# Performance work log

Measured on AMD Instinct MI355X. Metric: run time of the kernel, lower is better.

Reference implementation:

```python
import jax, jax.numpy as jnp
import numpy as np

N_BUCKET, EPB, K, TAU = 4, 4, 2, 1.0
C, H = 512, 1024
E = N_BUCKET * EPB
B, T = 2, 1024

def _l2norm(v):
    # matches F.normalize(dim=-1): v / max(||v||, 1e-12)
    return v / jnp.maximum(jnp.linalg.norm(v, axis=-1, keepdims=True), 1e-12)

def setup_inputs() -> dict:
    key = jax.random.key(0)
    ks = jax.random.split(key, 8)
    s = 1.0 / np.sqrt(C).astype(np.float32)
    sh = 1.0 / np.sqrt(H).astype(np.float32)
    return {
        "x": jax.random.normal(ks[0], (B, T, C), jnp.float32),
        "op_id": jax.random.randint(ks[1], (B, T), 0, N_BUCKET),
        "expert_key": jax.random.normal(ks[2], (N_BUCKET, EPB, C), jnp.float32) * s,
        "sW1": jax.random.normal(ks[3], (C, H), jnp.float32) * s,
        "sb1": jnp.zeros((H,), jnp.float32),
        "sW2": jax.random.normal(ks[4], (H, C), jnp.float32) * sh,
        "sb2": jnp.zeros((C,), jnp.float32),
        "eW1": jax.random.normal(ks[5], (E, C, H), jnp.float32) * s,
        "eb1": jnp.zeros((E, H), jnp.float32),
        "eW2": jax.random.normal(ks[6], (E, H, C), jnp.float32) * sh,
        "eb2": jnp.zeros((E, C), jnp.float32),
        "gate_logit": jnp.float32(-2.0),
    }

def reference(x, op_id, expert_key, sW1, sb1, sW2, sb2, eW1, eb1, eW2, eb2, gate_logit):
    Bb, Tt, Cc = x.shape
    # --- HierKVRouter ---
    bucket = jnp.clip(op_id, 0, N_BUCKET - 1)                 # (B,T)
    h_n = _l2norm(x)                                          # (B,T,C)
    keys = _l2norm(expert_key)                                # (nb,epb,C)
    keys_bt = keys[bucket]                                    # (B,T,epb,C) gather
    score = jnp.einsum('btc,btec->bte', h_n, keys_bt) / max(TAU, 1e-6)
    probs_local = jax.nn.softmax(score, axis=-1)              # (B,T,epb)
    topv, local = jax.lax.top_k(probs_local, K)               # (B,T,K)
    w = topv / (jnp.sum(topv, axis=-1, keepdims=True) + 1e-9) # combine weights
    gid = bucket[..., None] * EPB + local                     # (B,T,K) global ids
    # --- dispatch / expert MLP / combine ---
    flat_in = jnp.broadcast_to(x[:, :, None, :], (Bb, Tt, K, Cc)).reshape(-1, Cc)
    flat_gid = gid.reshape(-1)                                # (B*T*K,)
    flat_w = w.reshape(-1)                                    # (B*T*K,)
    out = jnp.zeros_like(flat_in)
    for e in range(E):  # fixed small expert count; masked dense = exact math of torch boolean-mask loop
        mask = (flat_gid == e)[:, None]
        h1 = jax.nn.relu(flat_in @ eW1[e] + eb1[e])
        oe = h1 @ eW2[e] + eb2[e]
        out = out + jnp.where(mask, oe * flat_w[:, None], 0.0)
    moe_out = out.reshape(Bb, Tt, K, Cc).sum(axis=2)          # (B,T,C)
    # --- shared dense FFN + gated combine ---
    dense = jax.nn.relu(x @ sW1 + sb1) @ sW2 + sb2
    y = dense + jax.nn.sigmoid(gate_logit) * moe_out
    return y
```

## Files before the change

### kernel.cpp

```cpp
#include <hip/hip_runtime.h>
#include <hip/hip_bf16.h>
#include <math.h>

#define C_DIM 512
#define H_DIM 1024
#define NTOK  2048
#define NSLOT 4096
#define NROWS 6144
#define MAXT128 64
#define MAXT64  112
#define NBG1 512

typedef __attribute__((ext_vector_type(8))) short short8;
typedef __attribute__((ext_vector_type(4))) float floatx4;
typedef __attribute__((address_space(3))) void as3_void;
typedef const __attribute__((address_space(1))) void as1_cvoid;

__device__ __forceinline__ void gload_lds16(const void* g, void* l){
  __builtin_amdgcn_global_load_lds((as1_cvoid*)g, (as3_void*)l, 16, 0, 0);
}

__device__ __forceinline__ unsigned short f2b(float f){
  unsigned int u = __float_as_uint(f);
  unsigned int r = (u + 0x7FFFu + ((u >> 16) & 1u)) >> 16;
  return (unsigned short)r;
}

__device__ __forceinline__ void transpose_tile(const float* __restrict__ in,
                                               unsigned short* __restrict__ out,
                                               int K, int N, int n0, int k0,
                                               int tid, float* tile){
  int tx = tid & 15, ty = tid >> 4;
  #pragma unroll
  for (int i = 0; i < 8; i++){
    int k = ty + 16 * i;
    float4 v = *reinterpret_cast<const float4*>(in + (size_t)(k0 + k) * N + n0 + tx * 4);
    tile[(4*tx + 0) * 129 + k] = v.x;
    tile[(4*tx + 1) * 129 + k] = v.y;
    tile[(4*tx + 2) * 129 + k] = v.z;
    tile[(4*tx + 3) * 129 + k] = v.w;
  }
  __syncthreads();
  int wt = tid & 31, wr = tid >> 5;
  #pragma unroll
  for (int i = 0; i < 8; i++){
    int n = wr + 8 * i;
    float4 v = *reinterpret_cast<const float4*>(&tile[n * 129 + 4 * wt]);
    ushort4 o;
    o.x = f2b(v.x); o.y = f2b(v.y); o.z = f2b(v.z); o.w = f2b(v.w);
    *reinterpret_cast<ushort4*>(out + (size_t)(n0 + n) * K + k0 + 4 * wt) = o;
  }
}

__global__ __launch_bounds__(256) void k_router(const float* __restrict__ x,
                                                const int* __restrict__ op_id,
                                                const float* __restrict__ ekey,
                                                unsigned short* __restrict__ Xb,
                                                int* __restrict__ gids,
                                                float* __restrict__ wv){
  int t = blockIdx.x * 4 + (threadIdx.x >> 6);
  int lane = threadIdx.x & 63;
  const float* xr = x + (size_t)t * C_DIM;
  {
    const float4* xr4 = reinterpret_cast<const float4*>(xr);
    float4 a = xr4[lane * 2], b = xr4[lane * 2 + 1];
    short8 o;
    o[0] = (short)f2b(a.x); o[1] = (short)f2b(a.y); o[2] = (short)f2b(a.z); o[3] = (short)f2b(a.w);
    o[4] = (short)f2b(b.x); o[5] = (short)f2b(b.y); o[6] = (short)f2b(b.z); o[7] = (short)f2b(b.w);
    *reinterpret_cast<short8*>(Xb + (size_t)t * C_DIM + lane * 8) = o;
  }
  float xs[8];
  float xn2 = 0.f;
  #pragma unroll
  for (int i = 0; i < 8; i++){ float v = xr[lane + 64*i]; xs[i] = v; xn2 += v*v; }
  #pragma unroll
  for (int o = 32; o; o >>= 1) xn2 += __shfl_xor(xn2, o, 64);
  int bucket = min(max(op_id[t], 0), 3);
  float xn = fmaxf(sqrtf(xn2), 1e-12f);
  float pr[4];
  #pragma unroll
  for (int e = 0; e < 4; e++){
    const float* kr = ekey + ((size_t)bucket * 4 + e) * C_DIM;
    float dot = 0.f, kn2 = 0.f;
    #pragma unroll
    for (int i = 0; i < 8; i++){ float kv = kr[lane + 64*i]; dot += xs[i]*kv; kn2 += kv*kv; }
    #pragma unroll
    for (int o = 32; o; o >>= 1){ dot += __shfl_xor(dot, o, 64); kn2 += __shfl_xor(kn2, o, 64); }
    float kn = fmaxf(sqrtf(kn2), 1e-12f);
    pr[e] = dot / (xn * kn);
  }
  float mx = fmaxf(fmaxf(pr[0], pr[1]), fmaxf(pr[2], pr[3]));
  float Z = 0.f;
  #pragma unroll
  for (int e = 0; e < 4; e++){ pr[e] = expf(pr[e] - mx); Z += pr[e]; }
  #pragma unroll
  for (int e = 0; e < 4; e++) pr[e] /= Z;
  int i0 = 0;
  #pragma unroll
  for (int e = 1; e < 4; e++) if (pr[e] > pr[i0]) i0 = e;
  int i1 = (i0 == 0) ? 1 : 0;
  #pragma unroll
  for (int e = 0; e < 4; e++) if (e != i0 && e != i1 && pr[e] > pr[i1]) i1 = e;
  float v0 = pr[i0], v1 = pr[i1];
  float wsum = v0 + v1 + 1e-9f;
  if (lane == 0){
    gids[2*t]   = bucket * 4 + i0;
    gids[2*t+1] = bucket * 4 + i1;
    wv[2*t]   = v0 / wsum;
    wv[2*t+1] = v1 / wsum;
  }
}

__global__ __launch_bounds__(256) void k_sortw1(const int* __restrict__ gids,
                                                const float* __restrict__ wv,
                                                const float* __restrict__ gate,
                                                const float* __restrict__ sW1,
                                                const float* __restrict__ eW1,
                                                unsigned short* __restrict__ sW1t,
                                                unsigned short* __restrict__ eW1t,
                                                int* __restrict__ inv,
                                                int* __restrict__ rowTok,
                                                float* __restrict__ rowW,
                                                int* __restrict__ tiles128,
                                                int* __restrict__ tiles64){
  __shared__ __align__(16) char smem[33280];
  const int bid = blockIdx.x;
  const int tid = threadIdx.x;

  if (bid == 0){
    int (*hist)[16] = (int(*)[16])smem;
    int* off = (int*)(smem + 16384);
    float sig = 1.f / (1.f + expf(-gate[0]));
    int h[16], g_[16];
    #pragma unroll
    for (int e = 0; e < 16; e++) h[e] = 0;
    int base = tid * 16;
    #pragma unroll
    for (int s = 0; s < 16; s++){ g_[s] = gids[base + s]; h[g_[s]]++; }
    #pragma unroll
    for (int e = 0; e < 16; e++) hist[tid][e] = h[e];
    __syncthreads();
    for (int d = 1; d < 256; d <<= 1){
      int v[16];
      if (tid >= d){
        #pragma unroll
        for (int e = 0; e < 16; e++) v[e] = hist[tid - d][e];
      }
      __syncthreads();
      if (tid >= d){
        #pragma unroll
        for (int e = 0; e < 16; e++) hist[tid][e] += v[e];
      }
      __syncthreads();
    }
    if (tid == 0){
      off[0] = 0;
      for (int e = 0; e < 16; e++) off[e+1] = off[e] + hist[255][e];
    }
    __syncthreads();
    int c[16];
    #pragma unroll
    for (int e = 0; e < 16; e++) c[e] = off[e] + hist[tid][e] - h[e];
    #pragma unroll
    for (int s = 0; s < 16; s++){
      int slot = base + s;
      int g = g_[s];
      int pos = c[g]++;
      inv[slot] = pos;
      rowTok[NTOK + pos] = slot >> 1;
      rowW[NTOK + pos] = sig * wv[slot];
    }
    for (int r = tid; r < NTOK; r += 256){ rowTok[r] = r; rowW[r] = 1.0f; }
    __syncthreads();
    if (tid == 0){
      int nt = 0;
      for (int r0 = 0; r0 < NTOK; r0 += 128){
        tiles128[nt*3] = r0; tiles128[nt*3+1] = 128; tiles128[nt*3+2] = 16; nt++;
      }
      for (int e = 0; e < 16; e++){
        int cc = off[e+1] - off[e];
        for (int r0 = 0; r0 < cc; r0 += 128){
          tiles128[nt*3] = NTOK + off[e] + r0;
          tiles128[nt*3+1] = min(128, cc - r0);
          tiles128[nt*3+2] = e;
          nt++;
        }
      }
      for (int i = nt; i < MAXT128; i++){ tiles128[i*3] = 0; tiles128[i*3+1] = 0; tiles128[i*3+2] = 0; }
      nt = 0;
      for (int r0 = 0; r0 < NTOK; r0 += 64){
        tiles64[nt*3] = r0; tiles64[nt*3+1] = 64; tiles64[nt*3+2] = 16; nt++;
      }
      for (int e = 0; e < 16; e++){
        int cc = off[e+1] - off[e];
        for (int r0 = 0; r0 < cc; r0 += 64){
          tiles64[nt*3] = NTOK + off[e] + r0;
          tiles64[nt*3+1] = min(64, cc - r0);
          tiles64[nt*3+2] = e;
          nt++;
        }
      }
      for (int i = nt; i < MAXT64; i++){ tiles64[i*3] = 0; tiles64[i*3+1] = 0; tiles64[i*3+2] = 0; }
    }
    return;
  }

  int tb = bid - 1;
  int mat = tb >> 6, tl = tb & 63;
  const float* in  = (mat < 16) ? eW1 + (size_t)mat * C_DIM * H_DIM : sW1;
  unsigned short* out = (mat < 16) ? eW1t + (size_t)mat * C_DIM * H_DIM : sW1t;
  transpose_tile(in, out, C_DIM, H_DIM, (tl & 15) * 64, (tl >> 4) * 128, tid, (float*)smem);
}

__global__ __launch_bounds__(256) void k_g1w2(const unsigned short* __restrict__ A,
                                              const unsigned short* __restrict__ BtE,
                                              const unsigned short* __restrict__ BtS,
                                              const float* __restrict__ biasE,
                                              const float* __restrict__ biasS,
                                              const int* __restrict__ rowTok,
                                              const int* __restrict__ tiles,
                                              unsigned short* __restrict__ outB,
                                              const float* __restrict__ sW2,
                                              const float* __restrict__ eW2,
                                              unsigned short* __restrict__ sW2t,
                                              unsigned short* __restrict__ eW2t){
  __shared__ __align__(16) char smem[33024];
  const int bx = blockIdx.x;
  const int tid = threadIdx.x;

  if (bx >= NBG1){
    int wi = bx - NBG1;
    int mat = wi >> 6, tl = wi & 63;
    const float* in  = (mat < 16) ? eW2 + (size_t)mat * H_DIM * C_DIM : sW2;
    unsigned short* out = (mat < 16) ? eW2t + (size_t)mat * H_DIM * C_DIM : sW2t;
    transpose_tile(in, out, H_DIM, C_DIM, (tl & 7) * 64, (tl >> 3) * 128, tid, (float*)smem);
    return;
  }

  constexpr int KDIM = C_DIM, NDIM = H_DIM;
  const int tileId = bx >> 3;
  const int rows = tiles[tileId*3+1];
  if (rows == 0) return;
  const int row0 = tiles[tileId*3];
  const int eid  = tiles[tileId*3+2];
  const unsigned short* Bt = (eid < 16) ? (BtE + (size_t)eid * NDIM * KDIM) : BtS;
  const float* bias = (eid < 16) ? (biasE + eid * NDIM) : biasS;
  const int n0 = (bx & 7) * 128;

  char* As = smem;
  char* Bs = smem + 16384;

  const int lane = tid & 63;
  const int wid = tid >> 6;
  const int wm = wid >> 1, wn = wid & 1;
  const int l15 = lane & 15, lhi = lane >> 4;

  int aRow[4], aOff[4], bRow[4], bOff[4];
  #pragma unroll
  for (int j = 0; j < 4; j++){
    int c = j * 256 + tid;
    int i = c >> 3, op = c & 7;
    int o = op ^ (i & 7);
    int ie = min(i, rows - 1);
    aRow[j] = rowTok[row0 + ie];
    aOff[j] = o * 8;
    bRow[j] = n0 + i;
    bOff[j] = o * 8;
  }

  floatx4 acc[4][4] = {};
  constexpr int NT = KDIM / 64;

  for (int kt = 0; kt < NT; ++kt){
    #pragma unroll
    for (int j = 0; j < 4; j++)
      gload_lds16(A + (size_t)aRow[j] * KDIM + kt * 64 + aOff[j],
                  As + (j * 256 + tid) * 16);
    #pragma unroll
    for (int j = 0; j < 4; j++)
      gload_lds16(Bt + (size_t)bRow[j] * KDIM + kt * 64 + bOff[j],
                  Bs + (j * 256 + tid) * 16);
    __syncthreads();
    #pragma unroll
    for (int kk = 0; kk < 2; ++kk){
      short8 a[4], b[4];
      #pragma unroll
      for (int m = 0; m < 4; m++){
        int rr = wm * 64 + m * 16 + l15;
        a[m] = *reinterpret_cast<const short8*>(
            As + rr * 128 + ((kk * 64 + lhi * 16) ^ ((rr & 7) << 4)));
      }
      #pragma unroll
      for (int n = 0; n < 4; n++){
        int rr = wn * 64 + n * 16 + l15;
        b[n] = *reinterpret_cast<const short8*>(
            Bs + rr * 128 + ((kk * 64 + lhi * 16) ^ ((rr & 7) << 4)));
      }
      #pragma unroll
      for (int m = 0; m < 4; m++)
        #pragma unroll
        for (int n = 0; n < 4; n++)
          acc[m][n] = __builtin_amdgcn_mfma_f32_16x16x32_bf16(a[m], b[n], acc[m][n], 0, 0, 0);
    }
    __syncthreads();
  }

  #pragma unroll
  for (int m = 0; m < 4; m++){
    #pragma unroll
    for (int n = 0; n < 4; n++){
      int gcol = n0 + wn * 64 + n * 16 + l15;
      float bv = bias[gcol];
      #pragma unroll
      for (int q = 0; q < 4; q++){
        int ri = wm * 64 + m * 16 + lhi * 4 + q;
        if (ri < rows){
          float v = fmaxf(acc[m][n][q] + bv, 0.f);
          outB[(size_t)(row0 + ri) * NDIM + gcol] = f2b(v);
        }
      }
    }
  }
}

template<int BMT, int KDIM, int NDIM>
__global__ __launch_bounds__(256) void k_gemm2(const unsigned short* __restrict__ A,
                                               const unsigned short* __restrict__ BtE,
                                               const unsigned short* __restrict__ BtS,
                                               const float* __restrict__ biasE,
                                               const float* __restrict__ biasS,
                                               const float* __restrict__ rowW,
                                               const int* __restrict__ tiles,
                                               float* __restrict__ outF){
  const int tileId = blockIdx.x;
  const int rows = tiles[tileId*3+1];
  if (rows == 0) return;
  const int row0 = tiles[tileId*3];
  const int eid  = tiles[tileId*3+2];
  const unsigned short* Bt = (eid < 16) ? (BtE + (size_t)eid * NDIM * KDIM) : BtS;
  const float* bias = (eid < 16) ? (biasE + eid * NDIM) : biasS;
  const int n0 = blockIdx.y * 128;

  constexpr int MREP = BMT / 32;
  constexpr int AISS = BMT * 8 / 256;

  __shared__ __align__(16) unsigned short As[2][BMT * 64];
  __shared__ __align__(16) unsigned short Bs[2][128 * 64];

  const int tid = threadIdx.x;
  const int lane = tid & 63;
  const int wid = tid >> 6;
  const int wm = wid >> 1, wn = wid & 1;
  const int l15 = lane & 15, lhi = lane >> 4;

  int aRow[AISS], aOff[AISS];
  #pragma unroll
  for (int j = 0; j < AISS; j++){
    int c = j * 256 + tid;
    int i = c >> 3, op = c & 7;
    int o = op ^ (i & 7);
    int ie = min(i, rows - 1);
    aRow[j] = row0 + ie;
    aOff[j] = o * 8;
  }
  int bRow[4], bOff[4];
  #pragma unroll
  for (int j = 0; j < 4; j++){
    int c = j * 256 + tid;
    int i = c >> 3, op = c & 7;
    int o = op ^ (i & 7);
    bRow[j] = n0 + i;
    bOff[j] = o * 8;
  }

  auto STAGE = [&](int buf, int kt){
    #pragma unroll
    for (int j = 0; j < AISS; j++)
      gload_lds16(A + (size_t)aRow[j] * KDIM + kt * 64 + aOff[j],
                  (char*)&As[buf][0] + (j * 256 + tid) * 16);
    #pragma unroll
    for (int j = 0; j < 4; j++)
      gload_lds16(Bt + (size_t)bRow[j] * KDIM + kt * 64 + bOff[j],
                  (char*)&Bs[buf][0] + (j * 256 + tid) * 16);
  };

  floatx4 acc[MREP][4] = {};
  constexpr int NT = KDIM / 64;

  STAGE(0, 0);
  for (int kt = 0; kt < NT; ++kt){
    const int cur = kt & 1;
    if (kt + 1 < NT){
      STAGE(cur ^ 1, kt + 1);
      asm volatile("s_waitcnt vmcnt(6)" ::: "memory");
    } else {
      asm volatile("s_waitcnt vmcnt(0)" ::: "memory");
    }
    __builtin_amdgcn_s_barrier();
    asm volatile("" ::: "memory");
    #pragma unroll
    for (int kk = 0; kk < 2; ++kk){
      short8 a[MREP], b[4];
      #pragma unroll
      for (int m = 0; m < MREP; m++){
        int rr = wm * (BMT/2) + m * 16 + l15;
        a[m] = *reinterpret_cast<const short8*>(
            (char*)&As[cur][0] + rr * 128 + ((kk * 64 + lhi * 16) ^ ((rr & 7) << 4)));
      }
      #pragma unroll
      for (int n = 0; n < 4; n++){
        int rr = wn * 64 + n * 16 + l15;
        b[n] = *reinterpret_cast<const short8*>(
            (char*)&Bs[cur][0] + rr * 128 + ((kk * 64 + lhi * 16) ^ ((rr & 7) << 4)));
      }
      #pragma unroll
      for (int m = 0; m < MREP; m++)
        #pragma unroll
        for (int n = 0; n < 4; n++)
          acc[m][n] = __builtin_amdgcn_mfma_f32_16x16x32_bf16(a[m], b[n], acc[m][n], 0, 0, 0);
    }
    asm volatile("" ::: "memory");
    __builtin_amdgcn_s_barrier();
  }

  #pragma unroll
  for (int m = 0; m < MREP; m++){
    #pragma unroll
    for (int n = 0; n < 4; n++){
      int gcol = n0 + wn * 64 + n * 16 + l15;
      float bv = bias[gcol];
      #pragma unroll
      for (int q = 0; q < 4; q++){
        int ri = wm * (BMT/2) + m * 16 + lhi * 4 + q;
        if (ri < rows){
          float v = (acc[m][n][q] + bv) * rowW[row0 + ri];
          outF[(size_t)(row0 + ri) * NDIM + gcol] = v;
        }
      }
    }
  }
}

__global__ __launch_bounds__(256) void k_combine(const float* __restrict__ O,
                                                 const int* __restrict__ inv,
                                                 float* __restrict__ y){
  int q = blockIdx.x * 256 + threadIdx.x;
  int t = q >> 7, c4 = q & 127;
  const float4* Of = reinterpret_cast<const float4*>(O);
  float4 d  = Of[(size_t)t * 128 + c4];
  int p0 = inv[2*t], p1 = inv[2*t+1];
  float4 o0 = Of[(size_t)(NTOK + p0) * 128 + c4];
  float4 o1 = Of[(size_t)(NTOK + p1) * 128 + c4];
  float4 r;
  r.x = d.x + o0.x + o1.x;
  r.y = d.y + o0.y + o1.y;
  r.z = d.z + o0.z + o1.z;
  r.w = d.w + o0.w + o1.w;
  reinterpret_cast<float4*>(y)[q] = r;
}

extern "C" void kernel_launch(void* const* d_in, const int* in_sizes, int n_in,
                              void* d_out, int out_size, void* d_ws, size_t ws_size,
                              hipStream_t stream){
  const float* x    = (const float*)d_in[0];
  const int*   opid = (const int*)d_in[1];
  const float* ekey = (const float*)d_in[2];
  const float* sW1  = (const float*)d_in[3];
  const float* sb1  = (const float*)d_in[4];
  const float* sW2  = (const float*)d_in[5];
  const float* sb2  = (const float*)d_in[6];
  const float* eW1  = (const float*)d_in[7];
  const float* eb1  = (const float*)d_in[8];
  const float* eW2  = (const float*)d_in[9];
  const float* eb2  = (const float*)d_in[10];
  const float* gate = (const float*)d_in[11];
  float* y = (float*)d_out;

  char* ws = (char*)d_ws;
  size_t off = 0;
  auto alloc = [&](size_t bytes) -> char* {
    char* p = ws + off; off += (bytes + 255) & ~(size_t)255; return p;
  };
  unsigned short* Xb   = (unsigned short*)alloc((size_t)NTOK * C_DIM * 2);
  unsigned short* sW1t = (unsigned short*)alloc((size_t)H_DIM * C_DIM * 2);
  unsigned short* sW2t = (unsigned short*)alloc((size_t)C_DIM * H_DIM * 2);
  unsigned short* eW1t = (unsigned short*)alloc((size_t)16 * H_DIM * C_DIM * 2);
  unsigned short* eW2t = (unsigned short*)alloc((size_t)16 * C_DIM * H_DIM * 2);
  unsigned short* H1   = (unsigned short*)alloc((size_t)NROWS * H_DIM * 2);
  float* O      = (float*)alloc((size_t)NROWS * C_DIM * 4);
  float* wv     = (float*)alloc((size_t)NSLOT * 4);
  int*   gids   = (int*)alloc((size_t)NSLOT * 4);
  int*   inv    = (int*)alloc((size_t)NSLOT * 4);
  int*   rowTok = (int*)alloc((size_t)NROWS * 4);
  float* rowW   = (float*)alloc((size_t)NROWS * 4);
  int*   tiles128 = (int*)alloc((size_t)MAXT128 * 3 * 4);
  int*   tiles64  = (int*)alloc((size_t)MAXT64 * 3 * 4);

  k_router<<<512, 256, 0, stream>>>(x, opid, ekey, Xb, gids, wv);
  k_sortw1<<<1 + 1088, 256, 0, stream>>>(gids, wv, gate, sW1, eW1, sW1t, eW1t,
                                         inv, rowTok, rowW, tiles128, tiles64);
  k_g1w2<<<NBG1 + 1088, 256, 0, stream>>>(Xb, eW1t, sW1t, eb1, sb1, rowTok, tiles128, H1,
                                          sW2, eW2, sW2t, eW2t);
  k_gemm2<64, H_DIM, C_DIM><<<dim3(MAXT64, C_DIM/128), 256, 0, stream>>>(
      H1, eW2t, sW2t, eb2, sb2, rowW, tiles64, O);
  k_combine<<<1024, 256, 0, stream>>>(O, inv, y);
}
```

Baseline: 79.58 us.

## Retile both GEMMs to 128-row tiles, widen gemm1 blocks, store gemm2 output as bf16

The first expert GEMM now runs 512-thread blocks that each cover 256 output columns instead of 128, with a block index remap that groups neighbouring column blocks of the same row tile. The weight-transpose blocks fused into that kernel are adapted to 512 threads. The second GEMM drops its 64-row double-buffered variant and reuses the 128-row tile list with a single-buffered loop, and it writes its output as bf16. The combine kernel then reads half the bytes. This cuts tile-list construction, the number of gemm2 blocks and intermediate traffic, but loses load/compute overlap in gemm2 and adds bf16 rounding error before the final sum.

```diff
diff --git a/kernel.cpp b/kernel.cpp
--- a/kernel.cpp
+++ b/kernel.cpp
@@ -8,8 +8,8 @@
 #define NSLOT 4096
 #define NROWS 6144
 #define MAXT128 64
-#define MAXT64  112
-#define NBG1 512
+#define NBG1 256
+#define NW2T 1088
 
 typedef __attribute__((ext_vector_type(8))) short short8;
 typedef __attribute__((ext_vector_type(4))) float floatx4;
@@ -24,6 +24,9 @@
   unsigned int u = __float_as_uint(f);
   unsigned int r = (u + 0x7FFFu + ((u >> 16) & 1u)) >> 16;
   return (unsigned short)r;
+}
+__device__ __forceinline__ float b2f(unsigned short s){
+  return __uint_as_float(((unsigned int)s) << 16);
 }
 
 __device__ __forceinline__ void transpose_tile(const float* __restrict__ in,
@@ -45,6 +48,32 @@
   #pragma unroll
   for (int i = 0; i < 8; i++){
     int n = wr + 8 * i;
+    float4 v = *reinterpret_cast<const float4*>(&tile[n * 129 + 4 * wt]);
+    ushort4 o;
+    o.x = f2b(v.x); o.y = f2b(v.y); o.z = f2b(v.z); o.w = f2b(v.w);
+    *reinterpret_cast<ushort4*>(out + (size_t)(n0 + n) * K + k0 + 4 * wt) = o;
+  }
+}
+
+__device__ __forceinline__ void transpose_tile512(const float* __restrict__ in,
+                                                  unsigned short* __restrict__ out,
+                                                  int K, int N, int n0, int k0,
+                                                  int tid, float* tile){
+  int tx = tid & 15, ty = tid >> 4;
+  #pragma unroll
+  for (int i = 0; i < 4; i++){
+    int k = ty + 32 * i;
+    float4 v = *reinterpret_cast<const float4*>(in + (size_t)(k0 + k) * N + n0 + tx * 4);
+    tile[(4*tx + 0) * 129 + k] = v.x;
+    tile[(4*tx + 1) * 129 + k] = v.y;
+    tile[(4*tx + 2) * 129 + k] = v.z;
+    tile[(4*tx + 3) * 129 + k] = v.w;
+  }
+  __syncthreads();
+  int wt = tid & 31, wr = tid >> 5;
+  #pragma unroll
+  for (int i = 0; i < 4; i++){
+    int n = wr + 16 * i;
     float4 v = *reinterpret_cast<const float4*>(&tile[n * 129 + 4 * wt]);
     ushort4 o;
     o.x = f2b(v.x); o.y = f2b(v.y); o.z = f2b(v.z); o.w = f2b(v.w);
@@ -121,8 +150,7 @@
                                                 int* __restrict__ inv,
                                                 int* __restrict__ rowTok,
                                                 float* __restrict__ rowW,
-                                                int* __restrict__ tiles128,
-                                                int* __restrict__ tiles64){
+                                                int* __restrict__ tiles128){
   __shared__ __align__(16) char smem[33280];
   const int bid = blockIdx.x;
   const int tid = threadIdx.x;
@@ -187,20 +215,6 @@
         }
       }
       for (int i = nt; i < MAXT128; i++){ tiles128[i*3] = 0; tiles128[i*3+1] = 0; tiles128[i*3+2] = 0; }
-      nt = 0;
-      for (int r0 = 0; r0 < NTOK; r0 += 64){
-        tiles64[nt*3] = r0; tiles64[nt*3+1] = 64; tiles64[nt*3+2] = 16; nt++;
-      }
-      for (int e = 0; e < 16; e++){
-        int cc = off[e+1] - off[e];
-        for (int r0 = 0; r0 < cc; r0 += 64){
-          tiles64[nt*3] = NTOK + off[e] + r0;
-          tiles64[nt*3+1] = min(64, cc - r0);
-          tiles64[nt*3+2] = e;
-          nt++;
-        }
-      }
-      for (int i = nt; i < MAXT64; i++){ tiles64[i*3] = 0; tiles64[i*3+1] = 0; tiles64[i*3+2] = 0; }
     }
     return;
   }
@@ -212,7 +226,7 @@
   transpose_tile(in, out, C_DIM, H_DIM, (tl & 15) * 64, (tl >> 4) * 128, tid, (float*)smem);
 }
 
-__global__ __launch_bounds__(256) void k_g1w2(const unsigned short* __restrict__ A,
+__global__ __launch_bounds__(512) void k_g1w2(const unsigned short* __restrict__ A,
                                               const unsigned short* __restrict__ BtE,
                                               const unsigned short* __restrict__ BtS,
                                               const float* __restrict__ biasE,
@@ -224,7 +238,7 @@
                                               const float* __restrict__ eW2,
                                               unsigned short* __restrict__ sW2t,
                                               unsigned short* __restrict__ eW2t){
-  __shared__ __align__(16) char smem[33024];
+  __shared__ __align__(16) char smem[49152];
   const int bx = blockIdx.x;
   const int tid = threadIdx.x;
 
@@ -233,53 +247,58 @@
     int mat = wi >> 6, tl = wi & 63;
     const float* in  = (mat < 16) ? eW2 + (size_t)mat * H_DIM * C_DIM : sW2;
     unsigned short* out = (mat < 16) ? eW2t + (size_t)mat * H_DIM * C_DIM : sW2t;
-    transpose_tile(in, out, H_DIM, C_DIM, (tl & 7) * 64, (tl >> 3) * 128, tid, (float*)smem);
+    transpose_tile512(in, out, H_DIM, C_DIM, (tl & 7) * 64, (tl >> 3) * 128, tid, (float*)smem);
     return;
   }
 
   constexpr int KDIM = C_DIM, NDIM = H_DIM;
-  const int tileId = bx >> 3;
+  const int tileId = (bx & 7) + 8 * (bx >> 5);
+  const int nb = (bx >> 3) & 3;
   const int rows = tiles[tileId*3+1];
   if (rows == 0) return;
   const int row0 = tiles[tileId*3];
   const int eid  = tiles[tileId*3+2];
   const unsigned short* Bt = (eid < 16) ? (BtE + (size_t)eid * NDIM * KDIM) : BtS;
   const float* bias = (eid < 16) ? (biasE + eid * NDIM) : biasS;
-  const int n0 = (bx & 7) * 128;
+  const int n0 = nb * 256;
 
   char* As = smem;
   char* Bs = smem + 16384;
 
   const int lane = tid & 63;
   const int wid = tid >> 6;
-  const int wm = wid >> 1, wn = wid & 1;
+  const int wm = wid >> 2, wn = wid & 3;
   const int l15 = lane & 15, lhi = lane >> 4;
 
-  int aRow[4], aOff[4], bRow[4], bOff[4];
-  #pragma unroll
-  for (int j = 0; j < 4; j++){
-    int c = j * 256 + tid;
+  int aRow[2], aOff[2], bRow[4], bOff[4];
+  #pragma unroll
+  for (int j = 0; j < 2; j++){
+    int c = j * 512 + tid;
     int i = c >> 3, op = c & 7;
     int o = op ^ (i & 7);
     int ie = min(i, rows - 1);
     aRow[j] = rowTok[row0 + ie];
     aOff[j] = o * 8;
+  }
+  #pragma unroll
+  for (int j = 0; j < 4; j++){
+    int c = j * 512 + tid;
+    int i = c >> 3, op = c & 7;
+    int o = op ^ (i & 7);
     bRow[j] = n0 + i;
     bOff[j] = o * 8;
   }
 
   floatx4 acc[4][4] = {};
-  constexpr int NT = KDIM / 64;
-
-  for (int kt = 0; kt < NT; ++kt){
-    #pragma unroll
-    for (int j = 0; j < 4; j++)
+  for (int kt = 0; kt < KDIM / 64; ++kt){
+    #pragma unroll
+    for (int j = 0; j < 2; j++)
       gload_lds16(A + (size_t)aRow[j] * KDIM + kt * 64 + aOff[j],
-                  As + (j * 256 + tid) * 16);
+                  As + (j * 512 + tid) * 16);
     #pragma unroll
     for (int j = 0; j < 4; j++)
       gload_lds16(Bt + (size_t)bRow[j] * KDIM + kt * 64 + bOff[j],
-                  Bs + (j * 256 + tid) * 16);
+                  Bs + (j * 512 + tid) * 16);
     __syncthreads();
     #pragma unroll
     for (int kk = 0; kk < 2; ++kk){
@@ -323,7 +342,6 @@
   }
 }
 
-template<int BMT, int KDIM, int NDIM>
 __global__ __launch_bounds__(256) void k_gemm2(const unsigned short* __restrict__ A,
                                                const unsigned short* __restrict__ BtE,
                                                const unsigned short* __restrict__ BtS,
@@ -331,21 +349,21 @@
                                                const float* __restrict__ biasS,
                                                const float* __restrict__ rowW,
                                                const int* __restrict__ tiles,
-                                               float* __restrict__ outF){
-  const int tileId = blockIdx.x;
+                                               unsigned short* __restrict__ outB){
+  constexpr int KDIM = H_DIM, NDIM = C_DIM;
+  const int bx = blockIdx.x;
+  const int tileId = (bx & 7) + 8 * (bx >> 5);
+  const int nb = (bx >> 3) & 3;
   const int rows = tiles[tileId*3+1];
   if (rows == 0) return;
   const int row0 = tiles[tileId*3];
   const int eid  = tiles[tileId*3+2];
   const unsigned short* Bt = (eid < 16) ? (BtE + (size_t)eid * NDIM * KDIM) : BtS;
   const float* bias = (eid < 16) ? (biasE + eid * NDIM) : biasS;
-  const int n0 = blockIdx.y * 128;
-
-  constexpr int MREP = BMT / 32;
-  constexpr int AISS = BMT * 8 / 256;
-
-  __shared__ __align__(16) unsigned short As[2][BMT * 64];
-  __shared__ __align__(16) unsigned short Bs[2][128 * 64];
+  const int n0 = nb * 128;
+
+  __shared__ __align__(16) unsigned short As[128 * 64];
+  __shared__ __align__(16) unsigned short Bs[128 * 64];
 
   const int tid = threadIdx.x;
   const int lane = tid & 63;
@@ -353,109 +371,87 @@
   const int wm = wid >> 1, wn = wid & 1;
   const int l15 = lane & 15, lhi = lane >> 4;
 
-  int aRow[AISS], aOff[AISS];
-  #pragma unroll
-  for (int j = 0; j < AISS; j++){
+  int aRow[4], aOff[4], bRow[4], bOff[4];
+  #pragma unroll
+  for (int j = 0; j < 4; j++){
     int c = j * 256 + tid;
     int i = c >> 3, op = c & 7;
     int o = op ^ (i & 7);
     int ie = min(i, rows - 1);
     aRow[j] = row0 + ie;
     aOff[j] = o * 8;
-  }
-  int bRow[4], bOff[4];
-  #pragma unroll
-  for (int j = 0; j < 4; j++){
-    int c = j * 256 + tid;
-    int i = c >> 3, op = c & 7;
-    int o = op ^ (i & 7);
     bRow[j] = n0 + i;
     bOff[j] = o * 8;
   }
 
-  auto STAGE = [&](int buf, int kt){
-    #pragma unroll
-    for (int j = 0; j < AISS; j++)
+  floatx4 acc[4][4] = {};
+  for (int kt = 0; kt < KDIM / 64; ++kt){
+    #pragma unroll
+    for (int j = 0; j < 4; j++)
       gload_lds16(A + (size_t)aRow[j] * KDIM + kt * 64 + aOff[j],
-                  (char*)&As[buf][0] + (j * 256 + tid) * 16);
+                  (char*)As + (j * 256 + tid) * 16);
     #pragma unroll
     for (int j = 0; j < 4; j++)
       gload_lds16(Bt + (size_t)bRow[j] * KDIM + kt * 64 + bOff[j],
-                  (char*)&Bs[buf][0] + (j * 256 + tid) * 16);
-  };
-
-  floatx4 acc[MREP][4] = {};
-  constexpr int NT = KDIM / 64;
-
-  STAGE(0, 0);
-  for (int kt = 0; kt < NT; ++kt){
-    const int cur = kt & 1;
-    if (kt + 1 < NT){
-      STAGE(cur ^ 1, kt + 1);
-      asm volatile("s_waitcnt vmcnt(6)" ::: "memory");
-    } else {
-      asm volatile("s_waitcnt vmcnt(0)" ::: "memory");
-    }
-    __builtin_amdgcn_s_barrier();
-    asm volatile("" ::: "memory");
+                  (char*)Bs + (j * 256 + tid) * 16);
+    __syncthreads();
     #pragma unroll
     for (int kk = 0; kk < 2; ++kk){
-      short8 a[MREP], b[4];
-      #pragma unroll
-      for (int m = 0; m < MREP; m++){
-        int rr = wm * (BMT/2) + m * 16 + l15;
+      short8 a[4], b[4];
+      #pragma unroll
+      for (int m = 0; m < 4; m++){
+        int rr = wm * 64 + m * 16 + l15;
         a[m] = *reinterpret_cast<const short8*>(
-            (char*)&As[cur][0] + rr * 128 + ((kk * 64 + lhi * 16) ^ ((rr & 7) << 4)));
+            (char*)As + rr * 128 + ((kk * 64 + lhi * 16) ^ ((rr & 7) << 4)));
       }
       #pragma unroll
       for (int n = 0; n < 4; n++){
         int rr = wn * 64 + n * 16 + l15;
         b[n] = *reinterpret_cast<const short8*>(
-            (char*)&Bs[cur][0] + rr * 128 + ((kk * 64 + lhi * 16) ^ ((rr & 7) << 4)));
-      }
-      #pragma unroll
-      for (int m = 0; m < MREP; m++)
+            (char*)Bs + rr * 128 + ((kk * 64 + lhi * 16) ^ ((rr & 7) << 4)));
+      }
+      #pragma unroll
+      for (int m = 0; m < 4; m++)
         #pragma unroll
         for (int n = 0; n < 4; n++)
           acc[m][n] = __builtin_amdgcn_mfma_f32_16x16x32_bf16(a[m], b[n], acc[m][n], 0, 0, 0);
     }
-    asm volatile("" ::: "memory");
-    __builtin_amdgcn_s_barrier();
-  }
-
-  #pragma unroll
-  for (int m = 0; m < MREP; m++){
+    __syncthreads();
+  }
+
+  #pragma unroll
+  for (int m = 0; m < 4; m++){
     #pragma unroll
     for (int n = 0; n < 4; n++){
       int gcol = n0 + wn * 64 + n * 16 + l15;
       float bv = bias[gcol];
       #pragma unroll
       for (int q = 0; q < 4; q++){
-        int ri = wm * (BMT/2) + m * 16 + lhi * 4 + q;
+        int ri = wm * 64 + m * 16 + lhi * 4 + q;
         if (ri < rows){
           float v = (acc[m][n][q] + bv) * rowW[row0 + ri];
-          outF[(size_t)(row0 + ri) * NDIM + gcol] = v;
+          outB[(size_t)(row0 + ri) * NDIM + gcol] = f2b(v);
         }
       }
     }
   }
 }
 
-__global__ __launch_bounds__(256) void k_combine(const float* __restrict__ O,
+__global__ __launch_bounds__(256) void k_combine(const unsigned short* __restrict__ O,
                                                  const int* __restrict__ inv,
                                                  float* __restrict__ y){
   int q = blockIdx.x * 256 + threadIdx.x;
   int t = q >> 7, c4 = q & 127;
-  const float4* Of = reinterpret_cast<const float4*>(O);
-  float4 d  = Of[(size_t)t * 128 + c4];
+  const ushort4* O4 = reinterpret_cast<const ushort4*>(O);
+  ushort4 d  = O4[(size_t)t * 128 + c4];
   int p0 = inv[2*t], p1 = inv[2*t+1];
-  float4 o0 = Of[(size_t)(NTOK + p0) * 128 + c4];
-  float4 o1 = Of[(size_t)(NTOK + p1) * 128 + c4];
+  ushort4 o0 = O4[(size_t)(NTOK + p0) * 128 + c4];
+  ushort4 o1 = O4[(size_t)(NTOK + p1) * 128 + c4];
   float4 r;
-  r.x = d.x + o0.x + o1.x;
-  r.y = d.y + o0.y + o1.y;
-  r.z = d.z + o0.z + o1.z;
-  r.w = d.w + o0.w + o1.w;
+  r.x = b2f(d.x) + b2f(o0.x) + b2f(o1.x);
+  r.y = b2f(d.y) + b2f(o0.y) + b2f(o1.y);
+  r.z = b2f(d.z) + b2f(o0.z) + b2f(o1.z);
+  r.w = b2f(d.w) + b2f(o0.w) + b2f(o1.w);
   reinterpret_cast<float4*>(y)[q] = r;
 }
 
@@ -487,21 +483,19 @@
   unsigned short* eW1t = (unsigned short*)alloc((size_t)16 * H_DIM * C_DIM * 2);
   unsigned short* eW2t = (unsigned short*)alloc((size_t)16 * C_DIM * H_DIM * 2);
   unsigned short* H1   = (unsigned short*)alloc((size_t)NROWS * H_DIM * 2);
-  float* O      = (float*)alloc((size_t)NROWS * C_DIM * 4);
+  unsigned short* O    = (unsigned short*)alloc((size_t)NROWS * C_DIM * 2);
   float* wv     = (float*)alloc((size_t)NSLOT * 4);
   int*   gids   = (int*)alloc((size_t)NSLOT * 4);
   int*   inv    = (int*)alloc((size_t)NSLOT * 4);
   int*   rowTok = (int*)alloc((size_t)NROWS * 4);
   float* rowW   = (float*)alloc((size_t)NROWS * 4);
   int*   tiles128 = (int*)alloc((size_t)MAXT128 * 3 * 4);
-  int*   tiles64  = (int*)alloc((size_t)MAXT64 * 3 * 4);
 
   k_router<<<512, 256, 0, stream>>>(x, opid, ekey, Xb, gids, wv);
   k_sortw1<<<1 + 1088, 256, 0, stream>>>(gids, wv, gate, sW1, eW1, sW1t, eW1t,
-                                         inv, rowTok, rowW, tiles128, tiles64);
-  k_g1w2<<<NBG1 + 1088, 256, 0, stream>>>(Xb, eW1t, sW1t, eb1, sb1, rowTok, tiles128, H1,
+                                         inv, rowTok, rowW, tiles128);
+  k_g1w2<<<NBG1 + NW2T, 512, 0, stream>>>(Xb, eW1t, sW1t, eb1, sb1, rowTok, tiles128, H1,
                                           sW2, eW2, sW2t, eW2t);
-  k_gemm2<64, H_DIM, C_DIM><<<dim3(MAXT64, C_DIM/128), 256, 0, stream>>>(
-      H1, eW2t, sW2t, eb2, sb2, rowW, tiles64, O);
+  k_gemm2<<<256, 256, 0, stream>>>(H1, eW2t, sW2t, eb2, sb2, rowW, tiles128, O);
   k_combine<<<1024, 256, 0, stream>>>(O, inv, y);
 }
```

New measurement: 85.28 us. 1.07x slower.

## Reschedule MoE pipeline stages to overlap dense and expert GEMMs with weight transposes

Applied to the files above, without the earlier changes.

Reorganizes the kernel chain so the W1 transposes run alongside the router, the shared dense GEMM1 runs alongside the sort and the W2 transposes, and the dense GEMM2 runs alongside the expert GEMM1. The expert GEMM2 now uses a separate kernel with 128-row tiles in place of the double-buffered 64-row gemm2. The goal is less dependency serialization and better fill of the GPU across stages. The cost is that the expert GEMM2 loses the double-buffered load pipeline, and the dense GEMM2 now waits on the same launch as the expert GEMM1.

```diff
diff --git a/kernel.cpp b/kernel.cpp
--- a/kernel.cpp
+++ b/kernel.cpp
@@ -7,9 +7,7 @@
 #define NTOK  2048
 #define NSLOT 4096
 #define NROWS 6144
-#define MAXT128 64
-#define MAXT64  112
-#define NBG1 512
+#define MAXTE 48
 
 typedef __attribute__((ext_vector_type(8))) short short8;
 typedef __attribute__((ext_vector_type(4))) float floatx4;
@@ -52,14 +50,119 @@
   }
 }
 
-__global__ __launch_bounds__(256) void k_router(const float* __restrict__ x,
-                                                const int* __restrict__ op_id,
-                                                const float* __restrict__ ekey,
-                                                unsigned short* __restrict__ Xb,
-                                                int* __restrict__ gids,
-                                                float* __restrict__ wv){
-  int t = blockIdx.x * 4 + (threadIdx.x >> 6);
-  int lane = threadIdx.x & 63;
+template<bool GATHER, bool RELU, bool OUTBF, bool WEIGHTED, int KDIM, int NDIM>
+__device__ __forceinline__ void gemm_tile(const unsigned short* __restrict__ A,
+                                          const unsigned short* __restrict__ Bt,
+                                          const float* __restrict__ bias,
+                                          const int* __restrict__ rowTok,
+                                          const float* __restrict__ rowW,
+                                          int row0, int rows, int n0,
+                                          int tid, char* smem,
+                                          unsigned short* __restrict__ outB,
+                                          float* __restrict__ outF){
+  char* As = smem;
+  char* Bs = smem + 16384;
+  const int lane = tid & 63;
+  const int wid = tid >> 6;
+  const int wm = wid >> 1, wn = wid & 1;
+  const int l15 = lane & 15, lhi = lane >> 4;
+
+  int aRow[4], aOff[4], bRow[4], bOff[4];
+  #pragma unroll
+  for (int j = 0; j < 4; j++){
+    int c = j * 256 + tid;
+    int i = c >> 3, op = c & 7;
+    int o = op ^ (i & 7);
+    int ie = min(i, rows - 1);
+    aRow[j] = GATHER ? rowTok[row0 + ie] : (row0 + ie);
+    aOff[j] = o * 8;
+    bRow[j] = n0 + i;
+    bOff[j] = o * 8;
+  }
+
+  floatx4 acc[4][4] = {};
+  for (int kt = 0; kt < KDIM / 64; ++kt){
+    #pragma unroll
+    for (int j = 0; j < 4; j++)
+      gload_lds16(A + (size_t)aRow[j] * KDIM + kt * 64 + aOff[j],
+                  As + (j * 256 + tid) * 16);
+    #pragma unroll
+    for (int j = 0; j < 4; j++)
+      gload_lds16(Bt + (size_t)bRow[j] * KDIM + kt * 64 + bOff[j],
+                  Bs + (j * 256 + tid) * 16);
+    __syncthreads();
+    #pragma unroll
+    for (int kk = 0; kk < 2; ++kk){
+      short8 a[4], b[4];
+      #pragma unroll
+      for (int m = 0; m < 4; m++){
+        int rr = wm * 64 + m * 16 + l15;
+        a[m] = *reinterpret_cast<const short8*>(
+            As + rr * 128 + ((kk * 64 + lhi * 16) ^ ((rr & 7) << 4)));
+      }
+      #pragma unroll
+      for (int n = 0; n < 4; n++){
+        int rr = wn * 64 + n * 16 + l15;
+        b[n] = *reinterpret_cast<const short8*>(
+            Bs + rr * 128 + ((kk * 64 + lhi * 16) ^ ((rr & 7) << 4)));
+      }
+      #pragma unroll
+      for (int m = 0; m < 4; m++)
+        #pragma unroll
+        for (int n = 0; n < 4; n++)
+          acc[m][n] = __builtin_amdgcn_mfma_f32_16x16x32_bf16(a[m], b[n], acc[m][n], 0, 0, 0);
+    }
+    __syncthreads();
+  }
+
+  #pragma unroll
+  for (int m = 0; m < 4; m++){
+    #pragma unroll
+    for (int n = 0; n < 4; n++){
+      int gcol = n0 + wn * 64 + n * 16 + l15;
+      float bv = bias[gcol];
+      #pragma unroll
+      for (int q = 0; q < 4; q++){
+        int ri = wm * 64 + m * 16 + lhi * 4 + q;
+        if (ri < rows){
+          float v = acc[m][n][q] + bv;
+          if constexpr (OUTBF){
+            if (RELU) v = fmaxf(v, 0.f);
+            outB[(size_t)(row0 + ri) * NDIM + gcol] = f2b(v);
+          } else {
+            if constexpr (WEIGHTED) v *= rowW[row0 + ri];
+            outF[(size_t)(row0 + ri) * NDIM + gcol] = v;
+          }
+        }
+      }
+    }
+  }
+}
+
+__global__ __launch_bounds__(256) void k_prep(const float* __restrict__ x,
+                                              const int* __restrict__ op_id,
+                                              const float* __restrict__ ekey,
+                                              const float* __restrict__ sW1,
+                                              const float* __restrict__ eW1,
+                                              unsigned short* __restrict__ Xb,
+                                              unsigned short* __restrict__ sW1t,
+                                              unsigned short* __restrict__ eW1t,
+                                              int* __restrict__ gids,
+                                              float* __restrict__ wv){
+  __shared__ __align__(16) float tile[64 * 129];
+  const int bid = blockIdx.x;
+  const int tid = threadIdx.x;
+
+  if (bid >= 512){
+    int tb = bid - 512;
+    int mat = tb >> 6, tl = tb & 63;
+    const float* in  = (mat < 16) ? eW1 + (size_t)mat * C_DIM * H_DIM : sW1;
+    unsigned short* out = (mat < 16) ? eW1t + (size_t)mat * C_DIM * H_DIM : sW1t;
+    transpose_tile(in, out, C_DIM, H_DIM, (tl & 15) * 64, (tl >> 4) * 128, tid, tile);
+    return;
+  }
+  int t = bid * 4 + (tid >> 6);
+  int lane = tid & 63;
   const float* xr = x + (size_t)t * C_DIM;
   {
     const float4* xr4 = reinterpret_cast<const float4*>(xr);
@@ -111,19 +214,22 @@
   }
 }
 
-__global__ __launch_bounds__(256) void k_sortw1(const int* __restrict__ gids,
-                                                const float* __restrict__ wv,
-                                                const float* __restrict__ gate,
-                                                const float* __restrict__ sW1,
-                                                const float* __restrict__ eW1,
-                                                unsigned short* __restrict__ sW1t,
-                                                unsigned short* __restrict__ eW1t,
-                                                int* __restrict__ inv,
-                                                int* __restrict__ rowTok,
-                                                float* __restrict__ rowW,
-                                                int* __restrict__ tiles128,
-                                                int* __restrict__ tiles64){
-  __shared__ __align__(16) char smem[33280];
+__global__ __launch_bounds__(256) void k_sg1d(const int* __restrict__ gids,
+                                              const float* __restrict__ wv,
+                                              const float* __restrict__ gate,
+                                              int* __restrict__ inv,
+                                              int* __restrict__ rowTok,
+                                              float* __restrict__ rowW,
+                                              int* __restrict__ tilesE,
+                                              const unsigned short* __restrict__ Xb,
+                                              const unsigned short* __restrict__ sW1t,
+                                              const float* __restrict__ sb1,
+                                              unsigned short* __restrict__ H1,
+                                              const float* __restrict__ sW2,
+                                              const float* __restrict__ eW2,
+                                              unsigned short* __restrict__ sW2t,
+                                              unsigned short* __restrict__ eW2t){
+  __shared__ __align__(16) char smem[33024];
   const int bid = blockIdx.x;
   const int tid = threadIdx.x;
 
@@ -170,275 +276,83 @@
       rowTok[NTOK + pos] = slot >> 1;
       rowW[NTOK + pos] = sig * wv[slot];
     }
-    for (int r = tid; r < NTOK; r += 256){ rowTok[r] = r; rowW[r] = 1.0f; }
     __syncthreads();
     if (tid == 0){
       int nt = 0;
-      for (int r0 = 0; r0 < NTOK; r0 += 128){
-        tiles128[nt*3] = r0; tiles128[nt*3+1] = 128; tiles128[nt*3+2] = 16; nt++;
-      }
       for (int e = 0; e < 16; e++){
         int cc = off[e+1] - off[e];
         for (int r0 = 0; r0 < cc; r0 += 128){
-          tiles128[nt*3] = NTOK + off[e] + r0;
-          tiles128[nt*3+1] = min(128, cc - r0);
-          tiles128[nt*3+2] = e;
+          tilesE[nt*3] = NTOK + off[e] + r0;
+          tilesE[nt*3+1] = min(128, cc - r0);
+          tilesE[nt*3+2] = e;
           nt++;
         }
       }
-      for (int i = nt; i < MAXT128; i++){ tiles128[i*3] = 0; tiles128[i*3+1] = 0; tiles128[i*3+2] = 0; }
-      nt = 0;
-      for (int r0 = 0; r0 < NTOK; r0 += 64){
-        tiles64[nt*3] = r0; tiles64[nt*3+1] = 64; tiles64[nt*3+2] = 16; nt++;
-      }
-      for (int e = 0; e < 16; e++){
-        int cc = off[e+1] - off[e];
-        for (int r0 = 0; r0 < cc; r0 += 64){
-          tiles64[nt*3] = NTOK + off[e] + r0;
-          tiles64[nt*3+1] = min(64, cc - r0);
-          tiles64[nt*3+2] = e;
-          nt++;
-        }
-      }
-      for (int i = nt; i < MAXT64; i++){ tiles64[i*3] = 0; tiles64[i*3+1] = 0; tiles64[i*3+2] = 0; }
+      for (int i = nt; i < MAXTE; i++){ tilesE[i*3] = 0; tilesE[i*3+1] = 0; tilesE[i*3+2] = 0; }
     }
     return;
   }
-
-  int tb = bid - 1;
+  if (bid <= 128){
+    int g = bid - 1;
+    gemm_tile<false, true, true, false, C_DIM, H_DIM>(
+        Xb, sW1t, sb1, nullptr, nullptr,
+        (g >> 3) * 128, 128, (g & 7) * 128, tid, smem, H1, nullptr);
+    return;
+  }
+  int tb = bid - 129;
   int mat = tb >> 6, tl = tb & 63;
-  const float* in  = (mat < 16) ? eW1 + (size_t)mat * C_DIM * H_DIM : sW1;
-  unsigned short* out = (mat < 16) ? eW1t + (size_t)mat * C_DIM * H_DIM : sW1t;
-  transpose_tile(in, out, C_DIM, H_DIM, (tl & 15) * 64, (tl >> 4) * 128, tid, (float*)smem);
-}
-
-__global__ __launch_bounds__(256) void k_g1w2(const unsigned short* __restrict__ A,
-                                              const unsigned short* __restrict__ BtE,
-                                              const unsigned short* __restrict__ BtS,
-                                              const float* __restrict__ biasE,
-                                              const float* __restrict__ biasS,
-                                              const int* __restrict__ rowTok,
-                                              const int* __restrict__ tiles,
-                                              unsigned short* __restrict__ outB,
-                                              const float* __restrict__ sW2,
-                                              const float* __restrict__ eW2,
-                                              unsigned short* __restrict__ sW2t,
-                                              unsigned short* __restrict__ eW2t){
+  const float* in  = (mat < 16) ? eW2 + (size_t)mat * H_DIM * C_DIM : sW2;
+  unsigned short* out = (mat < 16) ? eW2t + (size_t)mat * H_DIM * C_DIM : sW2t;
+  transpose_tile(in, out, H_DIM, C_DIM, (tl & 7) * 64, (tl >> 3) * 128, tid, (float*)smem);
+}
+
+__global__ __launch_bounds__(256) void k_g1e_g2d(const unsigned short* __restrict__ Xb,
+                                                 const unsigned short* __restrict__ eW1t,
+                                                 const float* __restrict__ eb1,
+                                                 const int* __restrict__ rowTok,
+                                                 const int* __restrict__ tilesE,
+                                                 unsigned short* __restrict__ H1,
+                                                 const unsigned short* __restrict__ sW2t,
+                                                 const float* __restrict__ sb2,
+                                                 float* __restrict__ O){
   __shared__ __align__(16) char smem[33024];
-  const int bx = blockIdx.x;
+  const int bid = blockIdx.x;
   const int tid = threadIdx.x;
 
-  if (bx >= NBG1){
-    int wi = bx - NBG1;
-    int mat = wi >> 6, tl = wi & 63;
-    const float* in  = (mat < 16) ? eW2 + (size_t)mat * H_DIM * C_DIM : sW2;
-    unsigned short* out = (mat < 16) ? eW2t + (size_t)mat * H_DIM * C_DIM : sW2t;
-    transpose_tile(in, out, H_DIM, C_DIM, (tl & 7) * 64, (tl >> 3) * 128, tid, (float*)smem);
+  if (bid < MAXTE * 8){
+    const int tileId = bid >> 3;
+    const int rows = tilesE[tileId*3+1];
+    if (rows == 0) return;
+    const int row0 = tilesE[tileId*3];
+    const int eid  = tilesE[tileId*3+2];
+    gemm_tile<true, true, true, false, C_DIM, H_DIM>(
+        Xb, eW1t + (size_t)eid * H_DIM * C_DIM, eb1 + eid * H_DIM, rowTok, nullptr,
+        row0, rows, (bid & 7) * 128, tid, smem, H1, nullptr);
     return;
   }
-
-  constexpr int KDIM = C_DIM, NDIM = H_DIM;
-  const int tileId = bx >> 3;
-  const int rows = tiles[tileId*3+1];
+  int g = bid - MAXTE * 8;
+  gemm_tile<false, false, false, false, H_DIM, C_DIM>(
+      H1, sW2t, sb2, nullptr, nullptr,
+      (g >> 2) * 128, 128, (g & 3) * 128, tid, smem, nullptr, O);
+}
+
+__global__ __launch_bounds__(256) void k_g2e(const unsigned short* __restrict__ H1,
+                                             const unsigned short* __restrict__ eW2t,
+                                             const float* __restrict__ eb2,
+                                             const float* __restrict__ rowW,
+                                             const int* __restrict__ tilesE,
+                                             float* __restrict__ O){
+  __shared__ __align__(16) char smem[33024];
+  const int bid = blockIdx.x;
+  const int tid = threadIdx.x;
+  const int tileId = bid >> 2;
+  const int rows = tilesE[tileId*3+1];
   if (rows == 0) return;
-  const int row0 = tiles[tileId*3];
-  const int eid  = tiles[tileId*3+2];
-  const unsigned short* Bt = (eid < 16) ? (BtE + (size_t)eid * NDIM * KDIM) : BtS;
-  const float* bias = (eid < 16) ? (biasE + eid * NDIM) : biasS;
-  const int n0 = (bx & 7) * 128;
-
-  char* As = smem;
-  char* Bs = smem + 16384;
-
-  const int lane = tid & 63;
-  const int wid = tid >> 6;
-  const int wm = wid >> 1, wn = wid & 1;
-  const int l15 = lane & 15, lhi = lane >> 4;
-
-  int aRow[4], aOff[4], bRow[4], bOff[4];
-  #pragma unroll
-  for (int j = 0; j < 4; j++){
-    int c = j * 256 + tid;
-    int i = c >> 3, op = c & 7;
-    int o = op ^ (i & 7);
-    int ie = min(i, rows - 1);
-    aRow[j] = rowTok[row0 + ie];
-    aOff[j] = o * 8;
-    bRow[j] = n0 + i;
-    bOff[j] = o * 8;
-  }
-
-  floatx4 acc[4][4] = {};
-  constexpr int NT = KDIM / 64;
-
-  for (int kt = 0; kt < NT; ++kt){
-    #pragma unroll
-    for (int j = 0; j < 4; j++)
-      gload_lds16(A + (size_t)aRow[j] * KDIM + kt * 64 + aOff[j],
-                  As + (j * 256 + tid) * 16);
-    #pragma unroll
-    for (int j = 0; j < 4; j++)
-      gload_lds16(Bt + (size_t)bRow[j] * KDIM + kt * 64 + bOff[j],
-                  Bs + (j * 256 + tid) * 16);
-    __syncthreads();
-    #pragma unroll
-    for (int kk = 0; kk < 2; ++kk){
-      short8 a[4], b[4];
-      #pragma unroll
-      for (int m = 0; m < 4; m++){
-        int rr = wm * 64 + m * 16 + l15;
-        a[m] = *reinterpret_cast<const short8*>(
-            As + rr * 128 + ((kk * 64 + lhi * 16) ^ ((rr & 7) << 4)));
-      }
-      #pragma unroll
-      for (int n = 0; n < 4; n++){
-        int rr = wn * 64 + n * 16 + l15;
-        b[n] = *reinterpret_cast<const short8*>(
-            Bs + rr * 128 + ((kk * 64 + lhi * 16) ^ ((rr & 7) << 4)));
-      }
-      #pragma unroll
-      for (int m = 0; m < 4; m++)
-        #pragma unroll
-        for (int n = 0; n < 4; n++)
-          acc[m][n] = __builtin_amdgcn_mfma_f32_16x16x32_bf16(a[m], b[n], acc[m][n], 0, 0, 0);
-    }
-    __syncthreads();
-  }
-
-  #pragma unroll
-  for (int m = 0; m < 4; m++){
-    #pragma unroll
-    for (int n = 0; n < 4; n++){
-      int gcol = n0 + wn * 64 + n * 16 + l15;
-      float bv = bias[gcol];
-      #pragma unroll
-      for (int q = 0; q < 4; q++){
-        int ri = wm * 64 + m * 16 + lhi * 4 + q;
-        if (ri < rows){
-          float v = fmaxf(acc[m][n][q] + bv, 0.f);
-          outB[(size_t)(row0 + ri) * NDIM + gcol] = f2b(v);
-        }
-      }
-    }
-  }
-}
-
-template<int BMT, int KDIM, int NDIM>
-__global__ __launch_bounds__(256) void k_gemm2(const unsigned short* __restrict__ A,
-                                               const unsigned short* __restrict__ BtE,
-                                               const unsigned short* __restrict__ BtS,
-                                               const float* __restrict__ biasE,
-                                               const float* __restrict__ biasS,
-                                               const float* __restrict__ rowW,
-                                               const int* __restrict__ tiles,
-                                               float* __restrict__ outF){
-  const int tileId = blockIdx.x;
-  const int rows = tiles[tileId*3+1];
-  if (rows == 0) return;
-  const int row0 = tiles[tileId*3];
-  const int eid  = tiles[tileId*3+2];
-  const unsigned short* Bt = (eid < 16) ? (BtE + (size_t)eid * NDIM * KDIM) : BtS;
-  const float* bias = (eid < 16) ? (biasE + eid * NDIM) : biasS;
-  const int n0 = blockIdx.y * 128;
-
-  constexpr int MREP = BMT / 32;
-  constexpr int AISS = BMT * 8 / 256;
-
-  __shared__ __align__(16) unsigned short As[2][BMT * 64];
-  __shared__ __align__(16) unsigned short Bs[2][128 * 64];
-
-  const int tid = threadIdx.x;
-  const int lane = tid & 63;
-  const int wid = tid >> 6;
-  const int wm = wid >> 1, wn = wid & 1;
-  const int l15 = lane & 15, lhi = lane >> 4;
-
-  int aRow[AISS], aOff[AISS];
-  #pragma unroll
-  for (int j = 0; j < AISS; j++){
-    int c = j * 256 + tid;
-    int i = c >> 3, op = c & 7;
-    int o = op ^ (i & 7);
-    int ie = min(i, rows - 1);
-    aRow[j] = row0 + ie;
-    aOff[j] = o * 8;
-  }
-  int bRow[4], bOff[4];
-  #pragma unroll
-  for (int j = 0; j < 4; j++){
-    int c = j * 256 + tid;
-    int i = c >> 3, op = c & 7;
-    int o = op ^ (i & 7);
-    bRow[j] = n0 + i;
-    bOff[j] = o * 8;
-  }
-
-  auto STAGE = [&](int buf, int kt){
-    #pragma unroll
-    for (int j = 0; j < AISS; j++)
-      gload_lds16(A + (size_t)aRow[j] * KDIM + kt * 64 + aOff[j],
-                  (char*)&As[buf][0] + (j * 256 + tid) * 16);
-    #pragma unroll
-    for (int j = 0; j < 4; j++)
-      gload_lds16(Bt + (size_t)bRow[j] * KDIM + kt * 64 + bOff[j],
-                  (char*)&Bs[buf][0] + (j * 256 + tid) * 16);
-  };
-
-  floatx4 acc[MREP][4] = {};
-  constexpr int NT = KDIM / 64;
-
-  STAGE(0, 0);
-  for (int kt = 0; kt < NT; ++kt){
-    const int cur = kt & 1;
-    if (kt + 1 < NT){
-      STAGE(cur ^ 1, kt + 1);
-      asm volatile("s_waitcnt vmcnt(6)" ::: "memory");
-    } else {
-      asm volatile("s_waitcnt vmcnt(0)" ::: "memory");
-    }
-    __builtin_amdgcn_s_barrier();
-    asm volatile("" ::: "memory");
-    #pragma unroll
-    for (int kk = 0; kk < 2; ++kk){
-      short8 a[MREP], b[4];
-      #pragma unroll
-      for (int m = 0; m < MREP; m++){
-        int rr = wm * (BMT/2) + m * 16 + l15;
-        a[m] = *reinterpret_cast<const short8*>(
-            (char*)&As[cur][0] + rr * 128 + ((kk * 64 + lhi * 16) ^ ((rr & 7) << 4)));
-      }
-      #pragma unroll
-      for (int n = 0; n < 4; n++){
-        int rr = wn * 64 + n * 16 + l15;
-        b[n] = *reinterpret_cast<const short8*>(
-            (char*)&Bs[cur][0] + rr * 128 + ((kk * 64 + lhi * 16) ^ ((rr & 7) << 4)));
-      }
-      #pragma unroll
-      for (int m = 0; m < MREP; m++)
-        #pragma unroll
-        for (int n = 0; n < 4; n++)
-          acc[m][n] = __builtin_amdgcn_mfma_f32_16x16x32_bf16(a[m], b[n], acc[m][n], 0, 0, 0);
-    }
-    asm volatile("" ::: "memory");
-    __builtin_amdgcn_s_barrier();
-  }
-
-  #pragma unroll
-  for (int m = 0; m < MREP; m++){
-    #pragma unroll
-    for (int n = 0; n < 4; n++){
-      int gcol = n0 + wn * 64 + n * 16 + l15;
-      float bv = bias[gcol];
-      #pragma unroll
-      for (int q = 0; q < 4; q++){
-        int ri = wm * (BMT/2) + m * 16 + lhi * 4 + q;
-        if (ri < rows){
-          float v = (acc[m][n][q] + bv) * rowW[row0 + ri];
-          outF[(size_t)(row0 + ri) * NDIM + gcol] = v;
-        }
-      }
-    }
-  }
+  const int row0 = tilesE[tileId*3];
+  const int eid  = tilesE[tileId*3+2];
+  gemm_tile<false, false, false, true, H_DIM, C_DIM>(
+      H1, eW2t + (size_t)eid * C_DIM * H_DIM, eb2 + eid * C_DIM, nullptr, rowW,
+      row0, rows, (bid & 3) * 128, tid, smem, nullptr, O);
 }
 
 __global__ __launch_bounds__(256) void k_combine(const float* __restrict__ O,
@@ -493,15 +407,13 @@
   int*   inv    = (int*)alloc((size_t)NSLOT * 4);
   int*   rowTok = (int*)alloc((size_t)NROWS * 4);
   float* rowW   = (float*)alloc((size_t)NROWS * 4);
-  int*   tiles128 = (int*)alloc((size_t)MAXT128 * 3 * 4);
-  int*   tiles64  = (int*)alloc((size_t)MAXT64 * 3 * 4);
-
-  k_router<<<512, 256, 0, stream>>>(x, opid, ekey, Xb, gids, wv);
-  k_sortw1<<<1 + 1088, 256, 0, stream>>>(gids, wv, gate, sW1, eW1, sW1t, eW1t,
-                                         inv, rowTok, rowW, tiles128, tiles64);
-  k_g1w2<<<NBG1 + 1088, 256, 0, stream>>>(Xb, eW1t, sW1t, eb1, sb1, rowTok, tiles128, H1,
-                                          sW2, eW2, sW2t, eW2t);
-  k_gemm2<64, H_DIM, C_DIM><<<dim3(MAXT64, C_DIM/128), 256, 0, stream>>>(
-      H1, eW2t, sW2t, eb2, sb2, rowW, tiles64, O);
+  int*   tilesE = (int*)alloc((size_t)MAXTE * 3 * 4);
+
+  k_prep<<<1600, 256, 0, stream>>>(x, opid, ekey, sW1, eW1, Xb, sW1t, eW1t, gids, wv);
+  k_sg1d<<<1 + 128 + 1088, 256, 0, stream>>>(gids, wv, gate, inv, rowTok, rowW, tilesE,
+                                             Xb, sW1t, sb1, H1, sW2, eW2, sW2t, eW2t);
+  k_g1e_g2d<<<MAXTE * 8 + 64, 256, 0, stream>>>(Xb, eW1t, eb1, rowTok, tilesE, H1,
+                                                sW2t, sb2, O);
+  k_g2e<<<MAXTE * 4, 256, 0, stream>>>(H1, eW2t, eb2, rowW, tilesE, O);
   k_combine<<<1024, 256, 0, stream>>>(O, inv, y);
 }
```

Measured after the change: 88.31 us. +11.0%, slower.
